# Kernel tuning notes

Hardware: AMD Instinct MI355X
Metric: run time of the kernel (lower is better)

Reference implementation:

```python
import jax, jax.numpy as jnp
import numpy as np

OUT_H, OUT_W = 512, 512
BATCH, CHANNELS = 64, 3


def setup_inputs() -> dict:
    key = jax.random.key(0)
    k1, k2 = jax.random.split(key)
    U = jax.random.normal(k1, (BATCH, OUT_H, OUT_W, CHANNELS), dtype=jnp.float32)
    theta = jax.random.normal(k2, (BATCH, 1), dtype=jnp.float32)
    return {"U": U, "theta": theta}


def reference(U, theta):
    B = U.shape[0]
    H, W = OUT_H, OUT_W
    # normalized sampling grid [H*W, 3] with homogeneous coordinate
    gx, gy = jnp.meshgrid(jnp.linspace(-1.0, 1.0, W), jnp.linspace(-1.0, 1.0, H))
    grid = jnp.stack([gx, gy, jnp.ones_like(gx)], axis=-1).reshape(H * W, 3)
    # rotation-only affine matrix [B, 2, 3]
    cos_t, sin_t, z = jnp.cos(theta), jnp.sin(theta), jnp.zeros_like(theta)
    rot = jnp.concatenate([cos_t, -sin_t, z, sin_t, cos_t, z], axis=1).reshape(B, 2, 3)
    # transformed source coords [B, H*W, 2]
    T_g = jnp.einsum('bij,nj->bni', rot, grid)
    x = (T_g[..., 0] + 1.0) * (W - 1) / 2.0
    y = (T_g[..., 1] + 1.0) * (H - 1) / 2.0
    x0f = jnp.floor(x).astype(jnp.int32)
    y0f = jnp.floor(y).astype(jnp.int32)
    x0 = jnp.clip(x0f, 0, W - 1)
    x1 = jnp.clip(x0f + 1, 0, W - 1)
    y0 = jnp.clip(y0f, 0, H - 1)
    y1 = jnp.clip(y0f + 1, 0, H - 1)
    # 4-corner gathers, batched: [B, H*W, C]
    gather = jax.vmap(lambda u, yy, xx: u[yy, xx])
    Ia = gather(U, y0, x0)
    Ib = gather(U, y1, x0)
    Ic = gather(U, y0, x1)
    Id = gather(U, y1, x1)
    x0_f, x1_f = x0.astype(jnp.float32), x1.astype(jnp.float32)
    y0_f, y1_f = y0.astype(jnp.float32), y1.astype(jnp.float32)
    wa = (x1_f - x) * (y1_f - y)
    wb = (x1_f - x) * (y - y0_f)
    wc = (x - x0_f) * (y1_f - y)
    wd = (x - x0_f) * (y - y0_f)
    out = (wa[..., None] * Ia + wb[..., None] * Ib
           + wc[..., None] * Ic + wd[..., None] * Id)
    return out.reshape(B, H, W, -1)
```

## Files before the change

kernel.cpp:

```cpp
#include <hip/hip_runtime.h>
#include <hip/hip_fp16.h>

#define OUT_H 512
#define OUT_W 512
#define BATCH 64
#define CHANS 3

#define WROWS 48
#define WPX   48
#define RSTRIDE 98
#define LSZ 4704
#define IDXMAX (LSZ - 149)

__global__ __launch_bounds__(256) void st_bilinear_kernel(
    const float* __restrict__ U,
    const float* __restrict__ theta,
    float* __restrict__ out)
{
    __shared__ __align__(16) unsigned int smf[LSZ];

    int blk  = blockIdx.x;
    int lblk = (blk & 7) * 2048 + (blk >> 3);

    int b  = lblk >> 8;
    int t  = lblk & 255;
    int i0 = (t >> 4) << 5;
    int j0 = (t & 15) << 5;

    int tid = threadIdx.x;

    float tt = theta[__builtin_amdgcn_readfirstlane(b)];
    float s, c;
    __sincosf(tt, &s, &c);

    const float scale = 2.0f / 511.0f;
    float gx0 = (float)j0 * scale - 1.0f;
    float gy0 = (float)i0 * scale - 1.0f;
    float xb0 = (c * gx0 - s * gy0 + 1.0f) * 255.5f;
    float yb0 = (s * gx0 + c * gy0 + 1.0f) * 255.5f;

    float xmin = xb0 + fminf(0.0f, 31.0f * c) + fminf(0.0f, -31.0f * s);
    float ymin = yb0 + fminf(0.0f, 31.0f * s) + fminf(0.0f,  31.0f * c);
    float xmax = xb0 + fmaxf(0.0f, 31.0f * c) + fmaxf(0.0f, -31.0f * s);
    float ymax = yb0 + fmaxf(0.0f, 31.0f * s) + fmaxf(0.0f,  31.0f * c);

    int bx0 = min(max((int)floorf(xmin), 0), OUT_W - 1);
    int by0 = min(max((int)floorf(ymin), 0), OUT_H - 1);
    int bx_load = min(bx0, OUT_W - WPX);
    int by_load = min(by0, OUT_H - WROWS);

    bool interior = (xmin >= 0.0f) & (xmax < 510.0f) &
                    (ymin >= 0.0f) & (ymax < 510.0f);

    const float* Ub = U + (size_t)b * (OUT_H * OUT_W * CHANS);
    const float* gb = Ub + ((size_t)by_load * OUT_W + bx_load) * CHANS;

    float4 va[9];
    bool origin = (b == 0) & (bx_load == 0) & (by_load == 0);
    if (!origin) {
#pragma unroll
        for (int k = 0; k < 9; ++k) {
            unsigned q = (unsigned)tid + 256u * k;
            unsigned r  = q / 48u;
            unsigned lx = q - r * 48u;
            va[k] = *(const float4*)(gb + (size_t)r * (OUT_W * CHANS) + lx * 3u - 1);
        }
    } else {
#pragma unroll
        for (int k = 0; k < 9; ++k) {
            unsigned q = (unsigned)tid + 256u * k;
            unsigned r  = q / 48u;
            unsigned lx = q - r * 48u;
            const float* p = gb + (size_t)r * (OUT_W * CHANS) + lx * 3u;
            float2 ab = *(const float2*)p;
            float  cc = p[2];
            va[k] = make_float4(0.0f, ab.x, ab.y, cc);
        }
    }
#pragma unroll
    for (int k = 0; k < 9; ++k) {
        unsigned q = (unsigned)tid + 256u * k;
        unsigned r  = q / 48u;
        unsigned lx = q - r * 48u;
        unsigned slot = RSTRIDE * r + lx;
        float4 v = va[k];
        __half2 hA = __floats2half2_rn(v.y, v.z);
        __half2 hB = __floats2half2_rn(v.w, 0.0f);
        smf[slot]      = *(const unsigned int*)&hA;
        smf[slot + 49] = *(const unsigned int*)&hB;
    }
    __syncthreads();

    int il = tid >> 3;
    int jb = (tid & 7) << 2;
    float xr = xb0 + c * (float)jb - s * (float)il;
    float yr = yb0 + s * (float)jb + c * (float)il;
    int Koff = by_load * RSTRIDE + bx_load;

    float o[12];
#pragma unroll
    for (int p = 0; p < 4; ++p) {
        float x = fmaf(c, (float)p, xr);
        float y = fmaf(s, (float)p, yr);
        int ix = __float2int_rd(x);
        int iy = __float2int_rd(y);
        float fx = x - (float)ix;
        float fy = y - (float)iy;

        int idx = iy * RSTRIDE + ix - Koff;
        if (!interior) idx = min(max(idx, 0), IDXMAX);

        const unsigned int* lp = smf + idx;
        unsigned iA0 = lp[0],   iA1 = lp[1];
        unsigned iB0 = lp[49],  iB1 = lp[50];
        unsigned iA2 = lp[98],  iA3 = lp[99];
        unsigned iB2 = lp[147], iB3 = lp[148];

        __half2 fx2 = __float2half2_rn(fx);
        __half2 fy2 = __float2half2_rn(fy);
        __half2 a01 = *(const __half2*)&iA0, c01 = *(const __half2*)&iA1;
        __half2 a2  = *(const __half2*)&iB0, c2  = *(const __half2*)&iB1;
        __half2 b01 = *(const __half2*)&iA2, d01 = *(const __half2*)&iA3;
        __half2 b2  = *(const __half2*)&iB2, d2  = *(const __half2*)&iB3;

        __half2 t01 = __hfma2(fx2, __hsub2(c01, a01), a01);
        __half2 t2  = __hfma2(fx2, __hsub2(c2,  a2),  a2);
        __half2 u01 = __hfma2(fx2, __hsub2(d01, b01), b01);
        __half2 u2  = __hfma2(fx2, __hsub2(d2,  b2),  b2);
        __half2 r01 = __hfma2(fy2, __hsub2(u01, t01), t01);
        __half2 r2  = __hfma2(fy2, __hsub2(u2,  t2),  t2);

        float v0 = __low2float(r01);
        float v1 = __high2float(r01);
        float v2 = __low2float(r2);
        if (!interior) {
            bool valid = ((unsigned)ix < 511u) & ((unsigned)iy < 511u);
            v0 = valid ? v0 : 0.0f;
            v1 = valid ? v1 : 0.0f;
            v2 = valid ? v2 : 0.0f;
        }
        o[p * 3 + 0] = v0;
        o[p * 3 + 1] = v1;
        o[p * 3 + 2] = v2;
    }

    float* po = out + (((size_t)b * OUT_H + (i0 + il)) * OUT_W + (j0 + jb)) * CHANS;
    ((float4*)po)[0] = make_float4(o[0], o[1], o[2],  o[3]);
    ((float4*)po)[1] = make_float4(o[4], o[5], o[6],  o[7]);
    ((float4*)po)[2] = make_float4(o[8], o[9], o[10], o[11]);
}

extern "C" void kernel_launch(void* const* d_in, const int* in_sizes, int n_in,
                              void* d_out, int out_size, void* d_ws, size_t ws_size,
                              hipStream_t stream) {
    const float* U     = (const float*)d_in[0];
    const float* theta = (const float*)d_in[1];
    float* out = (float*)d_out;

    int blocks = BATCH * (OUT_H / 32) * (OUT_W / 32);
    st_bilinear_kernel<<<blocks, 256, 0, stream>>>(U, theta, out);
}
```

Before: 103.0 us.

## Process two horizontal tiles per block, prefetching second window during first compute

Each block now handles a pair of adjacent 32x32 output tiles. The global loads for the second tile's source window are issued into registers before the first tile is computed, so their latency overlaps with the first tile's shared-memory interpolation and stores. The grid is halved and a second sync pair is added. This raises register pressure (two float4[9] staging arrays) and adds barriers, which could lower occupancy.

```diff
diff --git a/kernel.cpp b/kernel.cpp
--- a/kernel.cpp
+++ b/kernel.cpp
@@ -12,51 +12,32 @@
 #define LSZ 4704
 #define IDXMAX (LSZ - 149)
 
-__global__ __launch_bounds__(256) void st_bilinear_kernel(
-    const float* __restrict__ U,
-    const float* __restrict__ theta,
-    float* __restrict__ out)
-{
-    __shared__ __align__(16) unsigned int smf[LSZ];
-
-    int blk  = blockIdx.x;
-    int lblk = (blk & 7) * 2048 + (blk >> 3);
-
-    int b  = lblk >> 8;
-    int t  = lblk & 255;
-    int i0 = (t >> 4) << 5;
-    int j0 = (t & 15) << 5;
-
-    int tid = threadIdx.x;
-
-    float tt = theta[__builtin_amdgcn_readfirstlane(b)];
-    float s, c;
-    __sincosf(tt, &s, &c);
-
-    const float scale = 2.0f / 511.0f;
-    float gx0 = (float)j0 * scale - 1.0f;
-    float gy0 = (float)i0 * scale - 1.0f;
-    float xb0 = (c * gx0 - s * gy0 + 1.0f) * 255.5f;
-    float yb0 = (s * gx0 + c * gy0 + 1.0f) * 255.5f;
-
+struct Win {
+    float xb0, yb0;
+    int bx, by;
+    bool interior;
+};
+
+__device__ __forceinline__ Win make_win(float xb0, float yb0, float c, float s) {
     float xmin = xb0 + fminf(0.0f, 31.0f * c) + fminf(0.0f, -31.0f * s);
     float ymin = yb0 + fminf(0.0f, 31.0f * s) + fminf(0.0f,  31.0f * c);
     float xmax = xb0 + fmaxf(0.0f, 31.0f * c) + fmaxf(0.0f, -31.0f * s);
     float ymax = yb0 + fmaxf(0.0f, 31.0f * s) + fmaxf(0.0f,  31.0f * c);
-
+    Win w;
     int bx0 = min(max((int)floorf(xmin), 0), OUT_W - 1);
     int by0 = min(max((int)floorf(ymin), 0), OUT_H - 1);
-    int bx_load = min(bx0, OUT_W - WPX);
-    int by_load = min(by0, OUT_H - WROWS);
-
-    bool interior = (xmin >= 0.0f) & (xmax < 510.0f) &
-                    (ymin >= 0.0f) & (ymax < 510.0f);
-
-    const float* Ub = U + (size_t)b * (OUT_H * OUT_W * CHANS);
-    const float* gb = Ub + ((size_t)by_load * OUT_W + bx_load) * CHANS;
-
-    float4 va[9];
-    bool origin = (b == 0) & (bx_load == 0) & (by_load == 0);
+    w.bx = min(bx0, OUT_W - WPX);
+    w.by = min(by0, OUT_H - WROWS);
+    w.interior = (xmin >= 0.0f) & (xmax < 510.0f) &
+                 (ymin >= 0.0f) & (ymax < 510.0f);
+    w.xb0 = xb0; w.yb0 = yb0;
+    return w;
+}
+
+__device__ __forceinline__ void stage_load(const float* __restrict__ Ub,
+                                           const Win& w, int tid, bool origin,
+                                           float4 va[9]) {
+    const float* gb = Ub + ((size_t)w.by * OUT_W + w.bx) * CHANS;
     if (!origin) {
 #pragma unroll
         for (int k = 0; k < 9; ++k) {
@@ -77,6 +58,10 @@
             va[k] = make_float4(0.0f, ab.x, ab.y, cc);
         }
     }
+}
+
+__device__ __forceinline__ void stage_write(unsigned int* smf, int tid,
+                                            const float4 va[9]) {
 #pragma unroll
     for (int k = 0; k < 9; ++k) {
         unsigned q = (unsigned)tid + 256u * k;
@@ -89,13 +74,17 @@
         smf[slot]      = *(const unsigned int*)&hA;
         smf[slot + 49] = *(const unsigned int*)&hB;
     }
-    __syncthreads();
-
+}
+
+__device__ __forceinline__ void compute_store(const unsigned int* smf,
+                                              const Win& w, float c, float s,
+                                              int tid, float* __restrict__ po) {
     int il = tid >> 3;
     int jb = (tid & 7) << 2;
-    float xr = xb0 + c * (float)jb - s * (float)il;
-    float yr = yb0 + s * (float)jb + c * (float)il;
-    int Koff = by_load * RSTRIDE + bx_load;
+    float xr = w.xb0 + c * (float)jb - s * (float)il;
+    float yr = w.yb0 + s * (float)jb + c * (float)il;
+    int Koff = w.by * RSTRIDE + w.bx;
+    bool interior = w.interior;
 
     float o[12];
 #pragma unroll
@@ -144,10 +133,63 @@
         o[p * 3 + 2] = v2;
     }
 
-    float* po = out + (((size_t)b * OUT_H + (i0 + il)) * OUT_W + (j0 + jb)) * CHANS;
-    ((float4*)po)[0] = make_float4(o[0], o[1], o[2],  o[3]);
-    ((float4*)po)[1] = make_float4(o[4], o[5], o[6],  o[7]);
-    ((float4*)po)[2] = make_float4(o[8], o[9], o[10], o[11]);
+    float* pr = po + (size_t)il * (OUT_W * CHANS) + jb * CHANS;
+    ((float4*)pr)[0] = make_float4(o[0], o[1], o[2],  o[3]);
+    ((float4*)pr)[1] = make_float4(o[4], o[5], o[6],  o[7]);
+    ((float4*)pr)[2] = make_float4(o[8], o[9], o[10], o[11]);
+}
+
+__global__ __launch_bounds__(256) void st_bilinear_kernel(
+    const float* __restrict__ U,
+    const float* __restrict__ theta,
+    float* __restrict__ out)
+{
+    __shared__ __align__(16) unsigned int smf[LSZ];
+
+    int blk  = blockIdx.x;
+    int lp   = (blk & 7) * 1024 + (blk >> 3);
+    int b    = lp >> 7;
+    int pair = lp & 127;
+    int tr   = pair >> 3;
+    int i0   = tr << 5;
+    int j0A  = ((pair & 7) << 1) << 5;
+    int tid  = threadIdx.x;
+
+    float tt = theta[__builtin_amdgcn_readfirstlane(b)];
+    float s, c;
+    __sincosf(tt, &s, &c);
+
+    const float scale = 2.0f / 511.0f;
+    float gx0 = (float)j0A * scale - 1.0f;
+    float gy0 = (float)i0  * scale - 1.0f;
+    float xb0A = (c * gx0 - s * gy0 + 1.0f) * 255.5f;
+    float yb0A = (s * gx0 + c * gy0 + 1.0f) * 255.5f;
+
+    Win wA = make_win(xb0A, yb0A, c, s);
+    Win wB = make_win(xb0A + 32.0f * c, yb0A + 32.0f * s, c, s);
+
+    const float* Ub = U + (size_t)b * (OUT_H * OUT_W * CHANS);
+    bool b0 = (b == 0);
+
+    float4 va[9];
+    stage_load(Ub, wA, tid, b0 & (wA.bx == 0) & (wA.by == 0), va);
+    stage_write(smf, tid, va);
+
+    float4 vb[9];
+    stage_load(Ub, wB, tid, b0 & (wB.bx == 0) & (wB.by == 0), vb);
+
+    __syncthreads();
+
+    float* poA = out + (((size_t)b * OUT_H + i0) * OUT_W + j0A) * CHANS;
+    compute_store(smf, wA, c, s, tid, poA);
+
+    __syncthreads();
+
+    stage_write(smf, tid, vb);
+
+    __syncthreads();
+
+    compute_store(smf, wB, c, s, tid, poA + 32 * CHANS);
 }
 
 extern "C" void kernel_launch(void* const* d_in, const int* in_sizes, int n_in,
@@ -157,6 +199,6 @@
     const float* theta = (const float*)d_in[1];
     float* out = (float*)d_out;
 
-    int blocks = BATCH * (OUT_H / 32) * (OUT_W / 32);
+    int blocks = BATCH * (OUT_H / 32) * (OUT_W / 32) / 2;
     st_bilinear_kernel<<<blocks, 256, 0, stream>>>(U, theta, out);
 }
```

Result: slower. 112.5 us (+9.2%).

## Split block tile into per-wavefront 16x16 subtiles with private LDS windows

Applied to the files above, without the earlier changes.

Each of the four wavefronts now owns a 16x16 output subtile and stages its own 24x24 source window in a private LDS slice, so the block-wide __syncthreads is removed and each wave runs independently. Global loads are split into two batches interleaved with LDS stores. This removes block-level barrier stalls. In exchange, neighbouring windows overlap more, so more total global data is read, and no wave barrier is placed before LDS reads, which relies on lockstep execution within a wavefront.

```diff
diff --git a/kernel.cpp b/kernel.cpp
--- a/kernel.cpp
+++ b/kernel.cpp
@@ -6,28 +6,35 @@
 #define BATCH 64
 #define CHANS 3
 
-#define WROWS 48
-#define WPX   48
-#define RSTRIDE 98
-#define LSZ 4704
-#define IDXMAX (LSZ - 149)
+#define WIN   24
+#define RST   51
+#define BOFF  25
+#define WSLOT 1224
+#define IDXMAX (RST*22 + 22)
 
 __global__ __launch_bounds__(256) void st_bilinear_kernel(
     const float* __restrict__ U,
     const float* __restrict__ theta,
     float* __restrict__ out)
 {
-    __shared__ __align__(16) unsigned int smf[LSZ];
+    __shared__ __align__(16) unsigned int smf[4 * WSLOT];
 
     int blk  = blockIdx.x;
     int lblk = (blk & 7) * 2048 + (blk >> 3);
 
-    int b  = lblk >> 8;
-    int t  = lblk & 255;
-    int i0 = (t >> 4) << 5;
-    int j0 = (t & 15) << 5;
+    int b   = lblk >> 8;
+    int rem = lblk & 255;
+    int qr  = rem >> 4;
+    int qc  = rem & 15;
 
-    int tid = threadIdx.x;
+    int tid  = threadIdx.x;
+    int wid  = tid >> 6;
+    int lane = tid & 63;
+
+    int i0 = (qr << 5) + ((wid >> 1) << 4);
+    int j0 = (qc << 5) + ((wid & 1) << 4);
+
+    unsigned int* smw = smf + wid * WSLOT;
 
     float tt = theta[__builtin_amdgcn_readfirstlane(b)];
     float s, c;
@@ -39,63 +46,81 @@
     float xb0 = (c * gx0 - s * gy0 + 1.0f) * 255.5f;
     float yb0 = (s * gx0 + c * gy0 + 1.0f) * 255.5f;
 
-    float xmin = xb0 + fminf(0.0f, 31.0f * c) + fminf(0.0f, -31.0f * s);
-    float ymin = yb0 + fminf(0.0f, 31.0f * s) + fminf(0.0f,  31.0f * c);
-    float xmax = xb0 + fmaxf(0.0f, 31.0f * c) + fmaxf(0.0f, -31.0f * s);
-    float ymax = yb0 + fmaxf(0.0f, 31.0f * s) + fmaxf(0.0f,  31.0f * c);
+    float xmin = xb0 + fminf(0.0f, 15.0f * c) + fminf(0.0f, -15.0f * s);
+    float ymin = yb0 + fminf(0.0f, 15.0f * s) + fminf(0.0f,  15.0f * c);
+    float xmax = xb0 + fmaxf(0.0f, 15.0f * c) + fmaxf(0.0f, -15.0f * s);
+    float ymax = yb0 + fmaxf(0.0f, 15.0f * s) + fmaxf(0.0f,  15.0f * c);
 
     int bx0 = min(max((int)floorf(xmin), 0), OUT_W - 1);
     int by0 = min(max((int)floorf(ymin), 0), OUT_H - 1);
-    int bx_load = min(bx0, OUT_W - WPX);
-    int by_load = min(by0, OUT_H - WROWS);
+    int bx = min(bx0, OUT_W - WIN);
+    int by = min(by0, OUT_H - WIN);
 
     bool interior = (xmin >= 0.0f) & (xmax < 510.0f) &
                     (ymin >= 0.0f) & (ymax < 510.0f);
 
     const float* Ub = U + (size_t)b * (OUT_H * OUT_W * CHANS);
-    const float* gb = Ub + ((size_t)by_load * OUT_W + bx_load) * CHANS;
+    const float* gb = Ub + ((size_t)by * OUT_W + bx) * CHANS;
+    bool origin = (b == 0) & (bx == 0) & (by == 0);
 
-    float4 va[9];
-    bool origin = (b == 0) & (bx_load == 0) & (by_load == 0);
     if (!origin) {
+        float4 v0[5];
 #pragma unroll
-        for (int k = 0; k < 9; ++k) {
-            unsigned q = (unsigned)tid + 256u * k;
-            unsigned r  = q / 48u;
-            unsigned lx = q - r * 48u;
-            va[k] = *(const float4*)(gb + (size_t)r * (OUT_W * CHANS) + lx * 3u - 1);
+        for (int k = 0; k < 5; ++k) {
+            unsigned q = (unsigned)lane + 64u * k;
+            unsigned r = q / 24u, lx = q - r * 24u;
+            v0[k] = *(const float4*)(gb + (size_t)r * (OUT_W * CHANS) + lx * 3u - 1);
+        }
+#pragma unroll
+        for (int k = 0; k < 5; ++k) {
+            unsigned q = (unsigned)lane + 64u * k;
+            unsigned r = q / 24u, lx = q - r * 24u;
+            float4 v = v0[k];
+            __half2 hA = __floats2half2_rn(v.y, v.z);
+            __half2 hB = __floats2half2_rn(v.w, 0.0f);
+            unsigned slot = RST * r + lx;
+            smw[slot]        = *(const unsigned int*)&hA;
+            smw[slot + BOFF] = *(const unsigned int*)&hB;
+        }
+        float4 v1[4];
+#pragma unroll
+        for (int k = 0; k < 4; ++k) {
+            unsigned q = (unsigned)lane + 64u * (k + 5);
+            unsigned r = q / 24u, lx = q - r * 24u;
+            v1[k] = *(const float4*)(gb + (size_t)r * (OUT_W * CHANS) + lx * 3u - 1);
+        }
+#pragma unroll
+        for (int k = 0; k < 4; ++k) {
+            unsigned q = (unsigned)lane + 64u * (k + 5);
+            unsigned r = q / 24u, lx = q - r * 24u;
+            float4 v = v1[k];
+            __half2 hA = __floats2half2_rn(v.y, v.z);
+            __half2 hB = __floats2half2_rn(v.w, 0.0f);
+            unsigned slot = RST * r + lx;
+            smw[slot]        = *(const unsigned int*)&hA;
+            smw[slot + BOFF] = *(const unsigned int*)&hB;
         }
     } else {
 #pragma unroll
         for (int k = 0; k < 9; ++k) {
-            unsigned q = (unsigned)tid + 256u * k;
-            unsigned r  = q / 48u;
-            unsigned lx = q - r * 48u;
+            unsigned q = (unsigned)lane + 64u * k;
+            unsigned r = q / 24u, lx = q - r * 24u;
             const float* p = gb + (size_t)r * (OUT_W * CHANS) + lx * 3u;
             float2 ab = *(const float2*)p;
             float  cc = p[2];
-            va[k] = make_float4(0.0f, ab.x, ab.y, cc);
+            __half2 hA = __floats2half2_rn(ab.x, ab.y);
+            __half2 hB = __floats2half2_rn(cc, 0.0f);
+            unsigned slot = RST * r + lx;
+            smw[slot]        = *(const unsigned int*)&hA;
+            smw[slot + BOFF] = *(const unsigned int*)&hB;
         }
     }
-#pragma unroll
-    for (int k = 0; k < 9; ++k) {
-        unsigned q = (unsigned)tid + 256u * k;
-        unsigned r  = q / 48u;
-        unsigned lx = q - r * 48u;
-        unsigned slot = RSTRIDE * r + lx;
-        float4 v = va[k];
-        __half2 hA = __floats2half2_rn(v.y, v.z);
-        __half2 hB = __floats2half2_rn(v.w, 0.0f);
-        smf[slot]      = *(const unsigned int*)&hA;
-        smf[slot + 49] = *(const unsigned int*)&hB;
-    }
-    __syncthreads();
 
-    int il = tid >> 3;
-    int jb = (tid & 7) << 2;
-    float xr = xb0 + c * (float)jb - s * (float)il;
-    float yr = yb0 + s * (float)jb + c * (float)il;
-    int Koff = by_load * RSTRIDE + bx_load;
+    int il  = lane >> 2;
+    int jb2 = (lane & 3) << 2;
+    float xr = xb0 + c * (float)jb2 - s * (float)il;
+    float yr = yb0 + s * (float)jb2 + c * (float)il;
+    int Koff = by * RST + bx;
 
     float o[12];
 #pragma unroll
@@ -107,14 +132,14 @@
         float fx = x - (float)ix;
         float fy = y - (float)iy;
 
-        int idx = iy * RSTRIDE + ix - Koff;
+        int idx = iy * RST + ix - Koff;
         if (!interior) idx = min(max(idx, 0), IDXMAX);
 
-        const unsigned int* lp = smf + idx;
-        unsigned iA0 = lp[0],   iA1 = lp[1];
-        unsigned iB0 = lp[49],  iB1 = lp[50];
-        unsigned iA2 = lp[98],  iA3 = lp[99];
-        unsigned iB2 = lp[147], iB3 = lp[148];
+        const unsigned int* lp = smw + idx;
+        unsigned iA0 = lp[0],  iA1 = lp[1];
+        unsigned iB0 = lp[25], iB1 = lp[26];
+        unsigned iA2 = lp[51], iA3 = lp[52];
+        unsigned iB2 = lp[76], iB3 = lp[77];
 
         __half2 fx2 = __float2half2_rn(fx);
         __half2 fy2 = __float2half2_rn(fy);
@@ -144,7 +169,7 @@
         o[p * 3 + 2] = v2;
     }
 
-    float* po = out + (((size_t)b * OUT_H + (i0 + il)) * OUT_W + (j0 + jb)) * CHANS;
+    float* po = out + (((size_t)b * OUT_H + (i0 + il)) * OUT_W + (j0 + jb2)) * CHANS;
     ((float4*)po)[0] = make_float4(o[0], o[1], o[2],  o[3]);
     ((float4*)po)[1] = make_float4(o[4], o[5], o[6],  o[7]);
     ((float4*)po)[2] = make_float4(o[8], o[9], o[10], o[11]);
@@ -157,6 +182,6 @@
     const float* theta = (const float*)d_in[1];
     float* out = (float*)d_out;
 
-    int blocks = BATCH * (OUT_H / 32) * (OUT_W / 32);
+    int blocks = BATCH * 256;
     st_bilinear_kernel<<<blocks, 256, 0, stream>>>(U, theta, out);
 }
```

After: 127.8 us. +24.0%, slower.
